# Performance work log

Hardware: AMD Instinct MI355X
Metric: run time of the kernel (lower is better)

Reference implementation:

```python
import jax, jax.numpy as jnp
import numpy as np

B, S, D, H = 4, 2048, 512, 8
DH = D // H  # head dim = 64
NEG = -1000000.0


def setup_inputs() -> dict:
    key = jax.random.key(0)
    ks = jax.random.split(key, 13)
    s = 1.0 / np.sqrt(D)
    return {
        "Q": jax.random.normal(ks[0], (B, S, D), jnp.float32),
        "K": jax.random.normal(ks[1], (B, S, D), jnp.float32),
        "V": jax.random.normal(ks[2], (B, S, D), jnp.float32),
        "Wq": jax.random.normal(ks[3], (D, D), jnp.float32) * s,
        "bq": jnp.zeros((D,), jnp.float32),
        "Wk": jax.random.normal(ks[4], (D, D), jnp.float32) * s,
        "bk": jnp.zeros((D,), jnp.float32),
        "Wv": jax.random.normal(ks[5], (D, D), jnp.float32) * s,
        "bv": jnp.zeros((D,), jnp.float32),
        "Wo": jax.random.normal(ks[6], (D, D), jnp.float32) * s,
        "bo": jnp.zeros((D,), jnp.float32),
        "masked": jax.random.randint(ks[7], (B,), 1, S + 1, jnp.int64),
    }


def _heads(x):
    # [B,S,D] -> [B,H,S,DH]
    return x.reshape(B, S, H, DH).transpose(0, 2, 1, 3)


def reference(Q, K, V, Wq, bq, Wk, bk, Wv, bv, Wo, bo, masked):
    q = _heads(Q @ Wq.T + bq)
    k = _heads(K @ Wk.T + bk)
    v = _heads(V @ Wv.T + bv)
    scores = jnp.einsum("bhqd,bhkd->bhqk", q, k) / jnp.sqrt(jnp.asarray(DH, q.dtype))
    # valid-length key mask, per batch (same for every head and query row)
    key_mask = jnp.arange(S)[None, None, None, :] < masked[:, None, None, None]
    scores = jnp.where(key_mask, scores, jnp.asarray(NEG, scores.dtype))
    weights = jax.nn.softmax(scores, axis=-1)
    out = jnp.einsum("bhqk,bhkd->bhqd", weights, v)  # [B,H,S,DH]
    out = out.transpose(0, 2, 1, 3).reshape(B, S, D)
    return out @ Wo.T + bo
```

## Files before the change

kernel.cpp:

```cpp
#include <hip/hip_runtime.h>
#include <stdint.h>


typedef __attribute__((ext_vector_type(8))) short short8;
typedef __attribute__((ext_vector_type(4))) short short4v;
typedef __attribute__((ext_vector_type(4))) float f32x4;
typedef __attribute__((ext_vector_type(4))) unsigned short u16x4;

#define MFMA16(a, b, c) __builtin_amdgcn_mfma_f32_16x16x32_bf16(a, b, c, 0, 0, 0)

#define SCALE_LOG2 0.18033688011112042f
#define FIXED_M    32.0f
#define MASKED_E2  -200.0f

__device__ __forceinline__ unsigned short f2bf(float f) {
    unsigned int x = __float_as_uint(f);
    unsigned int r = (x + 0x7fffu + ((x >> 16) & 1u)) >> 16;
    return (unsigned short)r;
}
__device__ __forceinline__ short8 load8(const unsigned short* p) {
    return *reinterpret_cast<const short8*>(p);
}
__device__ __forceinline__ void gload_lds16(const unsigned short* g, unsigned short* l) {
    __builtin_amdgcn_global_load_lds(
        (const __attribute__((address_space(1))) unsigned int*)g,
        (__attribute__((address_space(3))) unsigned int*)l, 16, 0, 0);
}

__global__ __launch_bounds__(256)
void convert_bf16(const float4* __restrict__ Q, const float4* __restrict__ K,
                  const float4* __restrict__ V, const float4* __restrict__ Wq,
                  const float4* __restrict__ Wk, const float4* __restrict__ Wv,
                  const float4* __restrict__ Wo, u16x4* __restrict__ dst)
{
    const int n = 3407872;
    for (int i = blockIdx.x * 256 + threadIdx.x; i < n; i += gridDim.x * 256) {
        const float4* src; int off;
        if      (i < 1048576) { src = Q;  off = i; }
        else if (i < 2097152) { src = K;  off = i - 1048576; }
        else if (i < 3145728) { src = V;  off = i - 2097152; }
        else if (i < 3211264) { src = Wq; off = i - 3145728; }
        else if (i < 3276800) { src = Wk; off = i - 3211264; }
        else if (i < 3342336) { src = Wv; off = i - 3276800; }
        else                  { src = Wo; off = i - 3342336; }
        const float4 v = src[off];
        u16x4 r;
        r[0] = f2bf(v.x); r[1] = f2bf(v.y); r[2] = f2bf(v.z); r[3] = f2bf(v.w);
        dst[i] = r;
    }
}

__global__ __launch_bounds__(256)
void gemm_bf(const unsigned short* __restrict__ Aall,
             const unsigned short* __restrict__ Wall,
             const float* __restrict__ b0, const float* __restrict__ b1,
             const float* __restrict__ b2,
             void* __restrict__ outall, int out_mode)
{
    __shared__ unsigned short As[128 * 64];
    __shared__ unsigned short Bs[128 * 64];

    const int z = blockIdx.y;
    const unsigned short* A = Aall + (long)z * 4194304;
    const unsigned short* W = Wall + z * 262144;
    const float* bias = (z == 0) ? b0 : (z == 1) ? b1 : b2;
    void* out = (out_mode == 0)
        ? (void*)((unsigned short*)outall + (long)z * 4194304) : outall;

    const int f    = blockIdx.x;
    const int xcd  = f & 7;
    const int slot = f >> 3;
    const int col0 = (slot & 3) * 128;
    const int row0 = ((slot >> 2) * 8 + xcd) * 128;

    const int tid  = threadIdx.x;
    const int lane = tid & 63;
    const int w    = tid >> 6;
    const int quad = lane >> 4;
    const int nlow = lane & 15;
    const int wm   = w >> 1, wn = w & 1;

    const unsigned short* ag[4];
    const unsigned short* wg[4];
    unsigned short *la[4], *lb[4];
#pragma unroll
    for (int i = 0; i < 4; i++) {
        const int s = i * 256 + tid;
        const int r = s >> 3, kcl = s & 7;
        const int kg = kcl ^ (r & 7);
        ag[i] = A + (long)(row0 + r) * 512 + kg * 8;
        wg[i] = W + (long)(col0 + r) * 512 + kg * 8;
        const int ldso = i * 2048 + ((tid >> 6) << 9);
        la[i] = As + ldso;
        lb[i] = Bs + ldso;
    }

    f32x4 acc[4][4];
#pragma unroll
    for (int t = 0; t < 4; t++)
#pragma unroll
        for (int g = 0; g < 4; g++) acc[t][g] = (f32x4){0.f, 0.f, 0.f, 0.f};

    for (int k0 = 0; k0 < 512; k0 += 64) {
#pragma unroll
        for (int i = 0; i < 4; i++) {
            gload_lds16(ag[i] + k0, la[i]);
            gload_lds16(wg[i] + k0, lb[i]);
        }
        __syncthreads();

        short8 af[4][2], bf[4][2];
#pragma unroll
        for (int t = 0; t < 4; t++) {
            const int rowa = wm * 64 + t * 16 + nlow;
            const int rowb = wn * 64 + t * 16 + nlow;
#pragma unroll
            for (int kc = 0; kc < 2; kc++) {
                const int c = (kc * 4 + quad) ^ (nlow & 7);
                af[t][kc] = load8(&As[(rowa * 8 + c) * 8]);
                bf[t][kc] = load8(&Bs[(rowb * 8 + c) * 8]);
            }
        }
#pragma unroll
        for (int kc = 0; kc < 2; kc++)
#pragma unroll
            for (int t = 0; t < 4; t++)
#pragma unroll
                for (int g = 0; g < 4; g++)
                    acc[t][g] = MFMA16(af[t][kc], bf[g][kc], acc[t][g]);
        __syncthreads();
    }

#pragma unroll
    for (int g = 0; g < 4; g++) {
        const int j = col0 + wn * 64 + g * 16 + nlow;
        const float bj = bias[j];
#pragma unroll
        for (int t = 0; t < 4; t++) {
#pragma unroll
            for (int r = 0; r < 4; r++) {
                const int i = row0 + wm * 64 + t * 16 + quad * 4 + r;
                const float v = acc[t][g][r] + bj;
                if (out_mode == 0) {
                    const int b = i >> 11, s = i & 2047;
                    const int h = j >> 6, dh = j & 63;
                    ((unsigned short*)out)[(((b * 8 + h) * 2048) + s) * 64 + dh] = f2bf(v);
                } else {
                    ((float*)out)[(long)i * 512 + j] = v;
                }
            }
        }
    }
}

__global__ __launch_bounds__(256)
void attn_kernel(const unsigned short* __restrict__ qp,
                 const unsigned short* __restrict__ kp,
                 const unsigned short* __restrict__ vp,
                 const void* __restrict__ masked,
                 unsigned short* __restrict__ out)
{
    __shared__ unsigned short Ks[32][72];
    __shared__ unsigned short Vt[64][40];
    __shared__ unsigned short Ps[4][16][44];

    const int tid  = threadIdx.x;
    const int lane = tid & 63;
    const int w    = tid >> 6;
    const int quad = lane >> 4;
    const int nlow = lane & 15;

    const int b  = blockIdx.z;
    const int h  = blockIdx.y;
    const int q0 = blockIdx.x * 64 + w * 16;
    const long base = ((long)(b * 8 + h)) * 2048 * 64;

    const long long first = *reinterpret_cast<const long long*>(masked);
    int kmax;
    if ((first >> 32) != 0) kmax = reinterpret_cast<const int*>(masked)[b];
    else                    kmax = (int)reinterpret_cast<const long long*>(masked)[b];
    kmax = min(max(kmax, 1), 2048);

    const unsigned short* qrow = qp + base + (long)(q0 + nlow) * 64;
    const short8 aq0 = load8(qrow + quad * 8);
    const short8 aq1 = load8(qrow + 32 + quad * 8);

    short8 ones;
#pragma unroll
    for (int j = 0; j < 8; j++) ones[j] = (short)0x3F80;

    f32x4 o_acc[4], lacc;
#pragma unroll
    for (int vb = 0; vb < 4; vb++) o_acc[vb] = (f32x4){0.f, 0.f, 0.f, 0.f};
    lacc = (f32x4){0.f, 0.f, 0.f, 0.f};

    const int srow = tid >> 3;
    const int skk  = (tid & 7) * 8;
    const int kg   = srow >> 3;
    const int ko   = srow & 7;
    const int nkt  = (kmax + 31) >> 5;

    for (int kt = 0; kt < nkt; kt++) {
        const int k0 = kt * 32;
        *reinterpret_cast<short8*>(&Ks[srow][skk]) =
            load8(&kp[base + (long)(k0 + srow) * 64 + skk]);
        short8 vv = load8(&vp[base + (long)(k0 + srow) * 64 + skk]);
#pragma unroll
        for (int j = 0; j < 8; j++) {
            const int dh = skk + j;
            Vt[dh][((kg ^ ((dh >> 3) & 3)) << 3) + ko] = (unsigned short)vv[j];
        }
        __syncthreads();

        f32x4 sacc[2];
        sacc[0] = (f32x4){0.f, 0.f, 0.f, 0.f};
        sacc[1] = (f32x4){0.f, 0.f, 0.f, 0.f};
#pragma unroll
        for (int kb = 0; kb < 2; kb++) {
            short8 bk0 = load8(&Ks[kb * 16 + nlow][quad * 8]);
            short8 bk1 = load8(&Ks[kb * 16 + nlow][32 + quad * 8]);
            sacc[kb] = MFMA16(aq0, bk0, sacc[kb]);
            sacc[kb] = MFMA16(aq1, bk1, sacc[kb]);
        }

#pragma unroll
        for (int kb = 0; kb < 2; kb++) {
            const bool valid = (k0 + kb * 16 + nlow) < kmax;
#pragma unroll
            for (int r = 0; r < 4; r++) {
                const float e = valid ? fmaf(sacc[kb][r], SCALE_LOG2, -FIXED_M)
                                      : MASKED_E2;
                Ps[w][quad * 4 + r][kb * 16 + nlow] = f2bf(exp2f(e));
            }
        }
        __threadfence_block();

        const short4v apl = *reinterpret_cast<const short4v*>(&Ps[w][nlow][quad * 8]);
        const short4v aph = *reinterpret_cast<const short4v*>(&Ps[w][nlow][quad * 8 + 4]);
        short8 ap;
        ap[0] = apl[0]; ap[1] = apl[1]; ap[2] = apl[2]; ap[3] = apl[3];
        ap[4] = aph[0]; ap[5] = aph[1]; ap[6] = aph[2]; ap[7] = aph[3];

        lacc = MFMA16(ap, ones, lacc);
#pragma unroll
        for (int vb = 0; vb < 4; vb++) {
            const int dhr = vb * 16 + nlow;
            short8 bv = load8(&Vt[dhr][(quad ^ ((dhr >> 3) & 3)) << 3]);
            o_acc[vb] = MFMA16(ap, bv, o_acc[vb]);
        }
        __syncthreads();
    }

    float inv_l[4];
#pragma unroll
    for (int r = 0; r < 4; r++) inv_l[r] = 1.0f / lacc[r];
#pragma unroll
    for (int vb = 0; vb < 4; vb++) {
#pragma unroll
        for (int r = 0; r < 4; r++) {
            const int s   = q0 + quad * 4 + r;
            const int col = h * 64 + vb * 16 + nlow;
            out[(long)(b * 2048 + s) * 512 + col] = f2bf(o_acc[vb][r] * inv_l[r]);
        }
    }
}

extern "C" void kernel_launch(void* const* d_in, const int* in_sizes, int n_in,
                              void* d_out, int out_size, void* d_ws, size_t ws_size,
                              hipStream_t stream)
{
    const float4* Q  = (const float4*)d_in[0];
    const float4* K  = (const float4*)d_in[1];
    const float4* V  = (const float4*)d_in[2];
    const float4* Wq = (const float4*)d_in[3];
    const float*  bq = (const float*)d_in[4];
    const float4* Wk = (const float4*)d_in[5];
    const float*  bk = (const float*)d_in[6];
    const float4* Wv = (const float4*)d_in[7];
    const float*  bv = (const float*)d_in[8];
    const float4* Wo = (const float4*)d_in[9];
    const float*  bo = (const float*)d_in[10];
    const void*   masked = d_in[11];

    unsigned short* ws16 = (unsigned short*)d_ws;
    unsigned short* QKVb = ws16;
    unsigned short* Wb   = ws16 + 12582912;
    unsigned short* qp   = ws16 + 13631488;
    unsigned short* kp   = qp + 4194304;
    unsigned short* vp   = kp + 4194304;
    unsigned short* ao   = ws16;

    convert_bf16<<<2048, 256, 0, stream>>>(Q, K, V, Wq, Wk, Wv, Wo, (u16x4*)ws16);
    gemm_bf<<<dim3(256, 3), 256, 0, stream>>>(QKVb, Wb, bq, bk, bv, qp, 0);
    attn_kernel<<<dim3(32, 8, 4), 256, 0, stream>>>(qp, kp, vp, masked, ao);
    gemm_bf<<<dim3(256, 1), 256, 0, stream>>>(ao, Wb + 3 * 262144, bo, bo, bo,
                                              d_out, 1);
}
```

Before: 178.7 us.

## Double-buffer GEMM LDS loads and stage bf16 outputs for coalesced row-major stores

```diff
diff --git a/kernel.cpp b/kernel.cpp
--- a/kernel.cpp
+++ b/kernel.cpp
@@ -57,15 +57,12 @@
              const float* __restrict__ b2,
              void* __restrict__ outall, int out_mode)
 {
-    __shared__ unsigned short As[128 * 64];
-    __shared__ unsigned short Bs[128 * 64];
+    __shared__ unsigned short SM[32768];
 
     const int z = blockIdx.y;
     const unsigned short* A = Aall + (long)z * 4194304;
     const unsigned short* W = Wall + z * 262144;
     const float* bias = (z == 0) ? b0 : (z == 1) ? b1 : b2;
-    void* out = (out_mode == 0)
-        ? (void*)((unsigned short*)outall + (long)z * 4194304) : outall;
 
     const int f    = blockIdx.x;
     const int xcd  = f & 7;
@@ -82,7 +79,7 @@
 
     const unsigned short* ag[4];
     const unsigned short* wg[4];
-    unsigned short *la[4], *lb[4];
+    int ldso[4];
 #pragma unroll
     for (int i = 0; i < 4; i++) {
         const int s = i * 256 + tid;
@@ -90,9 +87,7 @@
         const int kg = kcl ^ (r & 7);
         ag[i] = A + (long)(row0 + r) * 512 + kg * 8;
         wg[i] = W + (long)(col0 + r) * 512 + kg * 8;
-        const int ldso = i * 2048 + ((tid >> 6) << 9);
-        la[i] = As + ldso;
-        lb[i] = Bs + ldso;
+        ldso[i] = i * 2048 + (w << 9);
     }
 
     f32x4 acc[4][4];
@@ -101,13 +96,25 @@
 #pragma unroll
         for (int g = 0; g < 4; g++) acc[t][g] = (f32x4){0.f, 0.f, 0.f, 0.f};
 
-    for (int k0 = 0; k0 < 512; k0 += 64) {
-#pragma unroll
-        for (int i = 0; i < 4; i++) {
-            gload_lds16(ag[i] + k0, la[i]);
-            gload_lds16(wg[i] + k0, lb[i]);
-        }
-        __syncthreads();
+#pragma unroll
+    for (int i = 0; i < 4; i++) {
+        gload_lds16(ag[i], SM + ldso[i]);
+        gload_lds16(wg[i], SM + 8192 + ldso[i]);
+    }
+
+    for (int it = 0; it < 8; ++it) {
+        __syncthreads();
+        if (it < 7) {
+            const int nb = (it + 1) & 1;
+            const int k0 = (it + 1) * 64;
+#pragma unroll
+            for (int i = 0; i < 4; i++) {
+                gload_lds16(ag[i] + k0, SM + nb * 16384 + ldso[i]);
+                gload_lds16(wg[i] + k0, SM + nb * 16384 + 8192 + ldso[i]);
+            }
+        }
+        const unsigned short* A_ = SM + (it & 1) * 16384;
+        const unsigned short* B_ = A_ + 8192;
 
         short8 af[4][2], bf[4][2];
 #pragma unroll
@@ -117,8 +124,8 @@
 #pragma unroll
             for (int kc = 0; kc < 2; kc++) {
                 const int c = (kc * 4 + quad) ^ (nlow & 7);
-                af[t][kc] = load8(&As[(rowa * 8 + c) * 8]);
-                bf[t][kc] = load8(&Bs[(rowb * 8 + c) * 8]);
+                af[t][kc] = load8(&A_[(rowa * 8 + c) * 8]);
+                bf[t][kc] = load8(&B_[(rowb * 8 + c) * 8]);
             }
         }
 #pragma unroll
@@ -128,27 +135,49 @@
 #pragma unroll
                 for (int g = 0; g < 4; g++)
                     acc[t][g] = MFMA16(af[t][kc], bf[g][kc], acc[t][g]);
-        __syncthreads();
-    }
-
-#pragma unroll
-    for (int g = 0; g < 4; g++) {
-        const int j = col0 + wn * 64 + g * 16 + nlow;
-        const float bj = bias[j];
-#pragma unroll
-        for (int t = 0; t < 4; t++) {
-#pragma unroll
-            for (int r = 0; r < 4; r++) {
-                const int i = row0 + wm * 64 + t * 16 + quad * 4 + r;
-                const float v = acc[t][g][r] + bj;
-                if (out_mode == 0) {
-                    const int b = i >> 11, s = i & 2047;
-                    const int h = j >> 6, dh = j & 63;
-                    ((unsigned short*)out)[(((b * 8 + h) * 2048) + s) * 64 + dh] = f2bf(v);
-                } else {
-                    ((float*)out)[(long)i * 512 + j] = v;
+    }
+
+    float bj[4];
+#pragma unroll
+    for (int g = 0; g < 4; g++) bj[g] = bias[col0 + wn * 64 + g * 16 + nlow];
+
+    if (out_mode == 1) {
+        float* out = (float*)outall;
+#pragma unroll
+        for (int g = 0; g < 4; g++) {
+            const int j = col0 + wn * 64 + g * 16 + nlow;
+#pragma unroll
+            for (int t = 0; t < 4; t++)
+#pragma unroll
+                for (int r = 0; r < 4; r++) {
+                    const int i = row0 + wm * 64 + t * 16 + quad * 4 + r;
+                    out[(long)i * 512 + j] = acc[t][g][r] + bj[g];
                 }
-            }
+        }
+        return;
+    }
+
+    unsigned short* out = (unsigned short*)outall + (long)z * 4194304;
+    for (int hf = 0; hf < 2; ++hf) {
+        __syncthreads();
+        if (wm == hf) {
+#pragma unroll
+            for (int t = 0; t < 4; t++)
+#pragma unroll
+                for (int g = 0; g < 4; g++)
+#pragma unroll
+                    for (int r = 0; r < 4; r++)
+                        SM[(t * 16 + quad * 4 + r) * 136 + wn * 64 + g * 16 + nlow] =
+                            f2bf(acc[t][g][r] + bj[g]);
+        }
+        __syncthreads();
+#pragma unroll
+        for (int c = 0; c < 4; c++) {
+            const int idx = c * 256 + tid;
+            const int row = idx >> 4, seg = idx & 15;
+            const long gi = row0 + hf * 64 + row;
+            *reinterpret_cast<short8*>(&out[gi * 512 + col0 + seg * 8]) =
+                *reinterpret_cast<const short8*>(&SM[row * 136 + seg * 8]);
         }
     }
 }
@@ -173,7 +202,7 @@
     const int b  = blockIdx.z;
     const int h  = blockIdx.y;
     const int q0 = blockIdx.x * 64 + w * 16;
-    const long base = ((long)(b * 8 + h)) * 2048 * 64;
+    const long base = (long)b * 1048576 + h * 64;
 
     const long long first = *reinterpret_cast<const long long*>(masked);
     int kmax;
@@ -181,7 +210,7 @@
     else                    kmax = (int)reinterpret_cast<const long long*>(masked)[b];
     kmax = min(max(kmax, 1), 2048);
 
-    const unsigned short* qrow = qp + base + (long)(q0 + nlow) * 64;
+    const unsigned short* qrow = qp + base + (long)(q0 + nlow) * 512;
     const short8 aq0 = load8(qrow + quad * 8);
     const short8 aq1 = load8(qrow + 32 + quad * 8);
 
@@ -203,8 +232,8 @@
     for (int kt = 0; kt < nkt; kt++) {
         const int k0 = kt * 32;
         *reinterpret_cast<short8*>(&Ks[srow][skk]) =
-            load8(&kp[base + (long)(k0 + srow) * 64 + skk]);
-        short8 vv = load8(&vp[base + (long)(k0 + srow) * 64 + skk]);
+            load8(&kp[base + (long)(k0 + srow) * 512 + skk]);
+        short8 vv = load8(&vp[base + (long)(k0 + srow) * 512 + skk]);
 #pragma unroll
         for (int j = 0; j < 8; j++) {
             const int dh = skk + j;
```

Measured after the change: 182.0 us. No clear change (+1.9%).
